# Kernel optimization log

Measured on AMD Instinct MI355X. Metric: run time of the kernel, lower is better.

Reference implementation:

```python
import jax, jax.numpy as jnp
import numpy as np
from jax import lax

DN = ('NHWC', 'HWIO', 'NHWC')

def conv2d(x, w, b):
    return lax.conv_general_dilated(x, w, (1, 1), 'SAME', dimension_numbers=DN) + b

def sdpa(q, k, v):
    # q,k,v: [B, C, L, D]; attend over L with feature dim D
    dk = jnp.asarray(q.shape[-1], dtype=q.dtype)
    scores = jnp.einsum('bcld,bcmd->bclm', q, k) / jnp.sqrt(dk)
    w = jax.nn.softmax(scores, axis=-1)
    return jnp.einsum('bclm,bcmd->bcld', w, v)

def setup_inputs() -> dict:
    key = jax.random.key(0)
    ks = jax.random.split(key, 8)
    B, T, F, N, C = 8, 512, 80, 64, 64
    s = 0.05
    return {
        'q': jax.random.normal(ks[0], (B, T, F, N), jnp.float32),
        'k': jax.random.normal(ks[1], (B, T, F, N), jnp.float32),
        'v': jax.random.normal(ks[2], (B, T, F, N), jnp.float32),
        'wq': jax.random.normal(ks[3], (3, 3, N, C), jnp.float32) * s,
        'bq': jnp.zeros((C,), jnp.float32),
        'wk': jax.random.normal(ks[4], (3, 3, N, C), jnp.float32) * s,
        'bk': jnp.zeros((C,), jnp.float32),
        'wv': jax.random.normal(ks[5], (3, 3, N, C), jnp.float32) * s,
        'bv': jnp.zeros((C,), jnp.float32),
        'wo': jax.random.normal(ks[6], (3, 3, 2 * C, N), jnp.float32) * s,
        'bo': jnp.zeros((N,), jnp.float32),
    }

def reference(q, k, v, wq, bq, wk, bk, wv, bv, wo, bo):
    cq = conv2d(q, wq, bq)  # [B,T,F,C]
    ck = conv2d(k, wk, bk)
    cv = conv2d(v, wv, bv)
    # 'freq' branch: [B,C,T,F], attention over T with feature dim F
    of = sdpa(jnp.transpose(cq, (0, 3, 1, 2)),
              jnp.transpose(ck, (0, 3, 1, 2)),
              jnp.transpose(cv, (0, 3, 1, 2)))  # [B,C,T,F]
    # 'time' branch: [B,C,F,T], attention over F with feature dim T
    ot = sdpa(jnp.transpose(cq, (0, 3, 2, 1)),
              jnp.transpose(ck, (0, 3, 2, 1)),
              jnp.transpose(cv, (0, 3, 2, 1)))  # [B,C,F,T]
    of = jnp.transpose(of, (0, 2, 3, 1))  # [B,T,F,C]
    ot = jnp.transpose(ot, (0, 3, 2, 1))  # [B,T,F,C]
    out = jnp.concatenate([ot, of], axis=-1)  # [B,T,F,2C]
    return conv2d(out, wo, bo)  # [B,T,F,N]
```

## Files before the change

kernel.cpp:

```cpp
#include <hip/hip_runtime.h>
#include <hip/hip_fp16.h>

#define TDIM 512
#define FDIM 80

typedef _Float16 f16x8 __attribute__((ext_vector_type(8)));
typedef _Float16 f16x4 __attribute__((ext_vector_type(4)));
typedef _Float16 f16x2 __attribute__((ext_vector_type(2)));
typedef float f32x4 __attribute__((ext_vector_type(4)));

__global__ __launch_bounds__(256) void k_prep_w(
    const float* __restrict__ wq, const float* __restrict__ wk,
    const float* __restrict__ wv, const float* __restrict__ wo,
    _Float16* __restrict__ wTq, _Float16* __restrict__ wTk,
    _Float16* __restrict__ wTv, _Float16* __restrict__ wTo)
{
  const int total = 3 * 36864 + 73728;
  for (int idx = blockIdx.x * 256 + threadIdx.x; idx < total; idx += gridDim.x * 256) {
    if (idx < 110592) {
      int sel = idx / 36864, r = idx - sel * 36864;
      int ci = r & 63, t2 = r >> 6, co = t2 & 63, kk = t2 >> 6;
      const float* src = (sel == 0) ? wq : (sel == 1) ? wk : wv;
      _Float16* dst = (sel == 0) ? wTq : (sel == 1) ? wTk : wTv;
      dst[r] = (_Float16)src[(kk * 64 + ci) * 64 + co];
    } else {
      int r = idx - 110592;
      int ci = r & 127, t2 = r >> 7, co = t2 & 63, kk = t2 >> 6;
      wTo[r] = (_Float16)wo[(kk * 128 + ci) * 64 + co];
    }
  }
}

__global__ __launch_bounds__(512) void k_conv_in3(
    const float* __restrict__ q, const float* __restrict__ k, const float* __restrict__ v,
    const float* __restrict__ wq, const float* __restrict__ wk, const float* __restrict__ wv,
    const _Float16* __restrict__ wTq, const _Float16* __restrict__ wTk, const _Float16* __restrict__ wTv,
    const float* __restrict__ bq, const float* __restrict__ bk, const float* __restrict__ bv,
    _Float16* __restrict__ yq, _Float16* __restrict__ yk, _Float16* __restrict__ yv)
{
  __shared__ __align__(16) _Float16 xs[328 * 72];
  const int bid = blockIdx.x;
  const int sel = bid >> 11, rest = bid & 2047;
  const float* x = (sel == 0) ? q : (sel == 1) ? k : v;
  const float* w = (sel == 0) ? wq : (sel == 1) ? wk : wv;
  const _Float16* wT = (sel == 0) ? wTq : (sel == 1) ? wTk : wTv;
  const float* bias = (sel == 0) ? bq : (sel == 1) ? bk : bv;
  _Float16* y = (sel == 0) ? yq : (sel == 1) ? yk : yv;

  const int xcd = rest & 7, i = rest >> 3;
  const int b = i >> 5, tp = i & 31;
  const int t0 = (xcd << 6) | (tp << 1);
  const int tid = threadIdx.x;
  const int wvv = tid >> 6, ln = tid & 63;
  const int tsel = wvv >> 2;
  const int lr = ln & 15, lg = ln >> 4;
  const int c0 = (wvv & 3) * 16;

  for (int idx = tid; idx < 328 * 16; idx += 512) {
    int r2 = idx >> 4, cq = idx & 15;
    int rr = r2 / 82, fi = r2 - rr * 82;
    int tt = t0 - 1 + rr, ff = fi - 1;
    f16x4 h;
    #pragma unroll
    for (int j = 0; j < 4; j++) h[j] = (_Float16)0.f;
    if (tt >= 0 && tt < TDIM && ff >= 0 && ff < FDIM) {
      float4 vv = *reinterpret_cast<const float4*>(x + (((b * TDIM + tt) * FDIM + ff) << 6) + cq * 4);
      h[0] = (_Float16)vv.x; h[1] = (_Float16)vv.y; h[2] = (_Float16)vv.z; h[3] = (_Float16)vv.w;
    }
    *reinterpret_cast<f16x4*>(&xs[r2 * 72 + cq * 4]) = h;
  }
  __syncthreads();

  float bvv = bias[c0 + lr];
  f32x4 acc[5];
  #pragma unroll
  for (int mt = 0; mt < 5; mt++)
    #pragma unroll
    for (int r = 0; r < 4; r++) acc[mt][r] = bvv;

  for (int ky = 0; ky < 3; ky++) {
    f16x8 wf[3][2];
    #pragma unroll
    for (int kx = 0; kx < 3; kx++)
      #pragma unroll
      for (int cc = 0; cc < 2; cc++) {
        if (wT) {
          wf[kx][cc] = *reinterpret_cast<const f16x8*>(
              wT + (((ky * 3 + kx) * 64 + c0 + lr) << 6) + cc * 32 + lg * 8);
        } else {
          const float* wp = w + ((ky * 3 + kx) * 64 + cc * 32 + lg * 8) * 64 + c0 + lr;
          #pragma unroll
          for (int j = 0; j < 8; j++) wf[kx][cc][j] = (_Float16)wp[j * 64];
        }
      }
    #pragma unroll
    for (int mt = 0; mt < 5; mt++) {
      #pragma unroll
      for (int kx = 0; kx < 3; kx++) {
        const _Float16* ap = &xs[((tsel + ky) * 82 + mt * 16 + lr + kx) * 72];
        #pragma unroll
        for (int cc = 0; cc < 2; cc++) {
          f16x8 af = *reinterpret_cast<const f16x8*>(ap + cc * 32 + lg * 8);
          acc[mt] = __builtin_amdgcn_mfma_f32_16x16x32_f16(af, wf[kx][cc], acc[mt], 0, 0, 0);
        }
      }
    }
  }

  __syncthreads();
  _Float16* yt = xs + tsel * 5632;
  const int c = c0 + lr;
  #pragma unroll
  for (int mt = 0; mt < 5; mt++) {
    f16x4 h;
    #pragma unroll
    for (int r = 0; r < 4; r++) h[r] = (_Float16)acc[mt][r];
    *reinterpret_cast<f16x4*>(&yt[c * 88 + mt * 16 + lg * 4]) = h;
  }
  __syncthreads();
  #pragma unroll
  for (int kk = 0; kk < 3; kk++) {
    int idx = tid + (kk << 9);
    if (idx < 1280) {
      int ts = idx >= 640, r2 = idx - ts * 640;
      int cc = r2 / 10, f8 = r2 - cc * 10;
      *reinterpret_cast<f16x8*>(y + ((size_t)(b * 64 + cc) * TDIM + t0 + ts) * FDIM + f8 * 8) =
          *reinterpret_cast<const f16x8*>(&xs[ts * 5632 + cc * 88 + f8 * 8]);
    }
  }
}

__global__ __launch_bounds__(512) void k_attn_freq(
    const _Float16* __restrict__ XQ, const _Float16* __restrict__ XK,
    const _Float16* __restrict__ XV, _Float16* __restrict__ CAT)
{
  __shared__ __align__(16) _Float16 Ks[64 * 104];
  __shared__ __align__(16) _Float16 Vt[96 * 72];
  __shared__ __align__(16) _Float16 Pl[8 * 16 * 72];

  const int bid = blockIdx.x;
  const int x8 = bid & 7, kk = bid >> 3;
  const int jj = kk & 7, tl = (kk >> 3) & 3, cc8 = kk >> 5;
  const int bc = x8 + cc8 * 64 + jj * 8;
  const int b = bc >> 6, c = bc & 63;
  const int t0 = tl * 128;
  const int tid = threadIdx.x;
  const int w8 = tid >> 6, ln = tid & 63;
  const int lr = ln & 15, lg = ln >> 4;
  const float qscale = 0.1118033988749895f;
  const float MFIX = 4.0f;

  const _Float16* Qg = XQ + (size_t)bc * 40960 + (size_t)t0 * 80;
  const _Float16* Kg = XK + (size_t)bc * 40960;
  const _Float16* Vg = XV + (size_t)bc * 40960;

  f16x8 qf[3];
  qf[0] = *reinterpret_cast<const f16x8*>(Qg + (w8 * 16 + lr) * 80 + lg * 8);
  qf[1] = *reinterpret_cast<const f16x8*>(Qg + (w8 * 16 + lr) * 80 + 32 + lg * 8);
  {
    f16x8 z;
    #pragma unroll
    for (int j = 0; j < 8; j++) z[j] = (_Float16)0.f;
    qf[2] = (lg < 2) ? *reinterpret_cast<const f16x8*>(Qg + (w8 * 16 + lr) * 80 + 64 + lg * 8) : z;
  }
  #pragma unroll
  for (int kc = 0; kc < 3; kc++)
    #pragma unroll
    for (int j = 0; j < 8; j++) qf[kc][j] = qf[kc][j] * (_Float16)qscale;

  if (tid < 192) {
    int row = tid / 3, cw = tid - row * 3;
    f16x8 z;
    #pragma unroll
    for (int j = 0; j < 8; j++) z[j] = (_Float16)0.f;
    *reinterpret_cast<f16x8*>(&Ks[row * 104 + 80 + cw * 8]) = z;
  }
  if (tid < 144) {
    int rr = tid / 9, cw = tid - rr * 9;
    int row = 80 + rr;
    f16x8 v;
    #pragma unroll
    for (int j = 0; j < 8; j++) v[j] = (row == 80) ? (_Float16)1.f : (_Float16)0.f;
    *reinterpret_cast<f16x8*>(&Vt[row * 72 + cw * 8]) = v;
  }

  const int vm = tid & 63;
  f16x8 kreg0, kreg1;
  f16x2 vreg[5];
  {
    int i0 = tid, r0 = i0 / 10, w0 = i0 - r0 * 10;
    kreg0 = *reinterpret_cast<const f16x8*>(Kg + r0 * 80 + w0 * 8);
    if (tid < 128) {
      int i1 = tid + 512, r1 = i1 / 10, w1 = i1 - r1 * 10;
      kreg1 = *reinterpret_cast<const f16x8*>(Kg + r1 * 80 + w1 * 8);
    }
    #pragma unroll
    for (int s = 0; s < 5; s++)
      vreg[s] = *reinterpret_cast<const f16x2*>(Vg + vm * 80 + (w8 + 8 * s) * 2);
  }

  f32x4 O[6];
  #pragma unroll
  for (int ft = 0; ft < 6; ft++)
    #pragma unroll
    for (int r = 0; r < 4; r++) O[ft][r] = 0.f;

  for (int kt = 0; kt < 8; kt++) {
    __syncthreads();
    {
      int i0 = tid, r0 = i0 / 10, w0 = i0 - r0 * 10;
      *reinterpret_cast<f16x8*>(&Ks[r0 * 104 + w0 * 8]) = kreg0;
      if (tid < 128) {
        int i1 = tid + 512, r1 = i1 / 10, w1 = i1 - r1 * 10;
        *reinterpret_cast<f16x8*>(&Ks[r1 * 104 + w1 * 8]) = kreg1;
      }
      #pragma unroll
      for (int s = 0; s < 5; s++) {
        int f2 = (w8 + 8 * s) * 2;
        Vt[f2 * 72 + vm]       = vreg[s][0];
        Vt[(f2 + 1) * 72 + vm] = vreg[s][1];
      }
    }
    if (kt < 7) {
      const _Float16* Kn = Kg + (kt + 1) * 64 * 80;
      const _Float16* Vn = Vg + (kt + 1) * 64 * 80;
      int i0 = tid, r0 = i0 / 10, w0 = i0 - r0 * 10;
      kreg0 = *reinterpret_cast<const f16x8*>(Kn + r0 * 80 + w0 * 8);
      if (tid < 128) {
        int i1 = tid + 512, r1 = i1 / 10, w1 = i1 - r1 * 10;
        kreg1 = *reinterpret_cast<const f16x8*>(Kn + r1 * 80 + w1 * 8);
      }
      #pragma unroll
      for (int s = 0; s < 5; s++)
        vreg[s] = *reinterpret_cast<const f16x2*>(Vn + vm * 80 + (w8 + 8 * s) * 2);
    }
    __syncthreads();

    f32x4 S[4];
    #pragma unroll
    for (int ms = 0; ms < 4; ms++)
      #pragma unroll
      for (int r = 0; r < 4; r++) S[ms][r] = 0.f;
    __builtin_amdgcn_s_setprio(1);
    #pragma unroll
    for (int kc = 0; kc < 3; kc++) {
      #pragma unroll
      for (int ms = 0; ms < 4; ms++) {
        f16x8 kf = *reinterpret_cast<const f16x8*>(&Ks[(ms * 16 + lr) * 104 + kc * 32 + lg * 8]);
        S[ms] = __builtin_amdgcn_mfma_f32_16x16x32_f16(qf[kc], kf, S[ms], 0, 0, 0);
      }
    }
    __builtin_amdgcn_s_setprio(0);

    _Float16* pw = &Pl[w8 * 16 * 72];
    #pragma unroll
    for (int r = 0; r < 4; r++) {
      int row = lg * 4 + r;
      #pragma unroll
      for (int ms = 0; ms < 4; ms++)
        pw[row * 72 + ((ms * 16 + lr) ^ (lg << 3))] = (_Float16)__expf(S[ms][r] - MFIX);
    }
    asm volatile("s_waitcnt lgkmcnt(0)" ::: "memory");
    const int sx = (lg ^ ((lr >> 2) & 3)) * 8;
    f16x8 pf0 = *reinterpret_cast<const f16x8*>(&pw[lr * 72 + sx]);
    f16x8 pf1 = *reinterpret_cast<const f16x8*>(&pw[lr * 72 + 32 + sx]);

    __builtin_amdgcn_s_setprio(1);
    #pragma unroll
    for (int ft = 0; ft < 6; ft++) {
      f16x8 vf0 = *reinterpret_cast<const f16x8*>(&Vt[(ft * 16 + lr) * 72 + lg * 8]);
      f16x8 vf1 = *reinterpret_cast<const f16x8*>(&Vt[(ft * 16 + lr) * 72 + 32 + lg * 8]);
      O[ft] = __builtin_amdgcn_mfma_f32_16x16x32_f16(pf0, vf0, O[ft], 0, 0, 0);
      O[ft] = __builtin_amdgcn_mfma_f32_16x16x32_f16(pf1, vf1, O[ft], 0, 0, 0);
    }
    __builtin_amdgcn_s_setprio(0);
  }

  float inv[4];
  #pragma unroll
  for (int r = 0; r < 4; r++) {
    float l = __shfl(O[5][r], lg << 4);
    inv[r] = 1.f / l;
  }
  #pragma unroll
  for (int r = 0; r < 4; r++) {
    int t = t0 + w8 * 16 + lg * 4 + r;
    size_t base = ((size_t)(b * 128 + 64 + c) * TDIM + t) * FDIM;
    #pragma unroll
    for (int ft = 0; ft < 5; ft++)
      CAT[base + ft * 16 + lr] = (_Float16)(O[ft][r] * inv[r]);
  }
}

__global__ __launch_bounds__(256) void k_attn_time(
    const _Float16* __restrict__ XQ, const _Float16* __restrict__ XK,
    const _Float16* __restrict__ XV, _Float16* __restrict__ CAT)
{
  __shared__ __align__(16) char smem[70400];
  _Float16* Qt  = (_Float16*)smem;
  _Float16* Kt  = Qt + 80 * 136;
  float*    Sld = (float*)(smem + 43520);
  _Float16* Pld = (_Float16*)smem;

  const int bid = blockIdx.x;
  const int b = bid >> 6, c = bid & 63;
  const int tid = threadIdx.x;
  const int wv = tid >> 6, ln = tid & 63;
  const int lr = ln & 15, lg = ln >> 4;
  const float tscale = 0.04419417382415922f;

  const _Float16* Qg = XQ + (size_t)bid * 40960;
  const _Float16* Kg = XK + (size_t)bid * 40960;
  const _Float16* Vg = XV + (size_t)bid * 40960;

  f32x4 sacc[7];
  #pragma unroll
  for (int i = 0; i < 7; i++)
    #pragma unroll
    for (int r = 0; r < 4; r++) sacc[i][r] = 0.f;

  for (int tc = 0; tc < 4; tc++) {
    __syncthreads();
    for (int idx = tid; idx < 640; idx += 256) {
      int t2 = idx / 10, f8 = idx - t2 * 10;
      int tg = tc * 128 + t2 * 2;
      f16x8 qa = *reinterpret_cast<const f16x8*>(Qg + (size_t)tg * 80 + f8 * 8);
      f16x8 qb = *reinterpret_cast<const f16x8*>(Qg + (size_t)(tg + 1) * 80 + f8 * 8);
      f16x8 ka = *reinterpret_cast<const f16x8*>(Kg + (size_t)tg * 80 + f8 * 8);
      f16x8 kb = *reinterpret_cast<const f16x8*>(Kg + (size_t)(tg + 1) * 80 + f8 * 8);
      #pragma unroll
      for (int j = 0; j < 8; j++) {
        int f = f8 * 8 + j;
        f16x2 qp; qp[0] = qa[j]; qp[1] = qb[j];
        f16x2 kp; kp[0] = ka[j]; kp[1] = kb[j];
        *reinterpret_cast<f16x2*>(&Qt[f * 136 + t2 * 2]) = qp;
        *reinterpret_cast<f16x2*>(&Kt[f * 136 + t2 * 2]) = kp;
      }
    }
    __syncthreads();
    #pragma unroll
    for (int i = 0; i < 7; i++) {
      int ti = wv * 7 + i;
      int te = ti < 25 ? ti : 24;
      int mi = te / 5, ni = te - mi * 5;
      #pragma unroll
      for (int kc = 0; kc < 4; kc++) {
        f16x8 aq = *reinterpret_cast<const f16x8*>(&Qt[(mi * 16 + lr) * 136 + kc * 32 + lg * 8]);
        f16x8 bk = *reinterpret_cast<const f16x8*>(&Kt[(ni * 16 + lr) * 136 + kc * 32 + lg * 8]);
        sacc[i] = __builtin_amdgcn_mfma_f32_16x16x32_f16(aq, bk, sacc[i], 0, 0, 0);
      }
    }
  }
  #pragma unroll
  for (int i = 0; i < 7; i++) {
    int ti = wv * 7 + i;
    if (ti < 25) {
      int mi = ti / 5, ni = ti - mi * 5;
      #pragma unroll
      for (int r = 0; r < 4; r++)
        Sld[(mi * 16 + lg * 4 + r) * 84 + ni * 16 + lr] = sacc[i][r] * tscale;
    }
  }
  __syncthreads();

  {
    const int fy = tid >> 4, gx = tid & 15;
    #pragma unroll
    for (int pass = 0; pass < 5; pass++) {
      int row = pass * 16 + fy;
      float s[5];
      #pragma unroll
      for (int j = 0; j < 5; j++) s[j] = Sld[row * 84 + gx + 16 * j];
      float mx = fmaxf(fmaxf(fmaxf(s[0], s[1]), fmaxf(s[2], s[3])), s[4]);
      #pragma unroll
      for (int sh = 1; sh < 16; sh <<= 1) mx = fmaxf(mx, __shfl_xor(mx, sh, 16));
      float e[5]; float ls = 0.f;
      #pragma unroll
      for (int j = 0; j < 5; j++) { e[j] = __expf(s[j] - mx); ls += e[j]; }
      #pragma unroll
      for (int sh = 1; sh < 16; sh <<= 1) ls += __shfl_xor(ls, sh, 16);
      float inv = 1.f / ls;
      #pragma unroll
      for (int j = 0; j < 5; j++)
        Pld[row * 104 + gx + 16 * j] = (_Float16)(e[j] * inv);
    }
    for (int idx = tid; idx < 240; idx += 256) {
      int row = idx / 3, cw = idx - row * 3;
      f16x8 z;
      #pragma unroll
      for (int j = 0; j < 8; j++) z[j] = (_Float16)0.f;
      *reinterpret_cast<f16x8*>(&Pld[row * 104 + 80 + cw * 8]) = z;
    }
  }
  __syncthreads();

  f16x8 pa[5][3];
  #pragma unroll
  for (int mi = 0; mi < 5; mi++)
    #pragma unroll
    for (int kc = 0; kc < 3; kc++)
      pa[mi][kc] = *reinterpret_cast<const f16x8*>(&Pld[(mi * 16 + lr) * 104 + kc * 32 + lg * 8]);

  _Float16* Ow = (_Float16*)(smem + 43520) + wv * (16 * 88);
  const size_t chbase = (size_t)(b * 128 + c) * TDIM * FDIM;

  #pragma unroll
  for (int j = 0; j < 8; j++) {
    int nt = wv * 8 + j;
    f16x8 vf[3];
    #pragma unroll
    for (int kc = 0; kc < 3; kc++) {
      if (kc < 2) {
        vf[kc] = *reinterpret_cast<const f16x8*>(Vg + (size_t)(nt * 16 + lr) * 80 + kc * 32 + lg * 8);
      } else {
        f16x8 z;
        #pragma unroll
        for (int q = 0; q < 8; q++) z[q] = (_Float16)0.f;
        vf[kc] = (lg < 2) ? *reinterpret_cast<const f16x8*>(Vg + (size_t)(nt * 16 + lr) * 80 + 64 + lg * 8) : z;
      }
    }
    f32x4 oacc[5];
    #pragma unroll
    for (int mi = 0; mi < 5; mi++)
      #pragma unroll
      for (int r = 0; r < 4; r++) oacc[mi][r] = 0.f;
    #pragma unroll
    for (int mi = 0; mi < 5; mi++)
      #pragma unroll
      for (int kc = 0; kc < 3; kc++)
        oacc[mi] = __builtin_amdgcn_mfma_f32_16x16x32_f16(pa[mi][kc], vf[kc], oacc[mi], 0, 0, 0);

    #pragma unroll
    for (int mi = 0; mi < 5; mi++) {
      f16x4 h;
      #pragma unroll
      for (int r = 0; r < 4; r++) h[r] = (_Float16)oacc[mi][r];
      *reinterpret_cast<f16x4*>(&Ow[lr * 88 + mi * 16 + lg * 4]) = h;
    }
    asm volatile("s_waitcnt lgkmcnt(0)" ::: "memory");
    size_t basec = chbase + (size_t)(nt * 16) * FDIM;
    #pragma unroll
    for (int k = 0; k < 3; k++) {
      int idx = ln + (k << 6);
      if (idx < 160) {
        int tl2 = idx / 10, f8 = idx - tl2 * 10;
        *reinterpret_cast<f16x8*>(CAT + basec + tl2 * 80 + f8 * 8) =
            *reinterpret_cast<const f16x8*>(&Ow[tl2 * 88 + f8 * 8]);
      }
    }
  }
}

__global__ __launch_bounds__(256) void k_conv_out(
    const _Float16* __restrict__ x, const float* __restrict__ w,
    const _Float16* __restrict__ wT,
    const float* __restrict__ bias, float* __restrict__ out)
{
  __shared__ __align__(16) _Float16 xs[246 * 72];
  const int bid = blockIdx.x;
  const int xcd = bid & 7, i = bid >> 3;
  const int b = i >> 6, t = (xcd << 6) | (i & 63);
  const int tid = threadIdx.x;
  const int wv = tid >> 6, ln = tid & 63;
  const int lr = ln & 15, lg = ln >> 4;
  const int c0 = wv * 16;

  float bv = bias[c0 + lr];
  f32x4 acc[5];
  #pragma unroll
  for (int mt = 0; mt < 5; mt++)
    #pragma unroll
    for (int r = 0; r < 4; r++) acc[mt][r] = bv;

  const _Float16* xb = x + (size_t)b * 128 * TDIM * FDIM;

  for (int h = 0; h < 2; h++) {
    __syncthreads();
    for (int idx = tid; idx < 384; idx += 256) {
      int cch = idx & 63, sk = idx >> 6;
      int ky = sk >> 1, side = sk & 1;
      xs[(ky * 82 + side * 81) * 72 + cch] = (_Float16)0.f;
    }
    #pragma unroll
    for (int k = 0; k < 8; k++) {
      int idx = tid + (k << 8);
      if (idx < 1920) {
        int cch = idx & 63, rest = idx >> 6;
        int ky = rest / 10, f8 = rest - ky * 10;
        int tt = t + ky - 1;
        f16x8 hh;
        #pragma unroll
        for (int j = 0; j < 8; j++) hh[j] = (_Float16)0.f;
        if (tt >= 0 && tt < TDIM)
          hh = *reinterpret_cast<const f16x8*>(xb + ((size_t)(h * 64 + cch) * TDIM + tt) * FDIM + f8 * 8);
        #pragma unroll
        for (int j = 0; j < 8; j++)
          xs[(ky * 82 + f8 * 8 + j + 1) * 72 + cch] = hh[j];
      }
    }
    __syncthreads();

    for (int ky = 0; ky < 3; ky++) {
      f16x8 wf[3][2];
      #pragma unroll
      for (int kx = 0; kx < 3; kx++)
        #pragma unroll
        for (int cc = 0; cc < 2; cc++) {
          if (wT) {
            wf[kx][cc] = *reinterpret_cast<const f16x8*>(
                wT + (((ky * 3 + kx) * 64 + c0 + lr) << 7) + h * 64 + cc * 32 + lg * 8);
          } else {
            const float* wp = w + ((ky * 3 + kx) * 128 + h * 64 + cc * 32 + lg * 8) * 64 + c0 + lr;
            #pragma unroll
            for (int j = 0; j < 8; j++) wf[kx][cc][j] = (_Float16)wp[j * 64];
          }
        }
      #pragma unroll
      for (int mt = 0; mt < 5; mt++) {
        #pragma unroll
        for (int kx = 0; kx < 3; kx++) {
          const _Float16* ap = &xs[(ky * 82 + mt * 16 + lr + kx) * 72];
          #pragma unroll
          for (int cc = 0; cc < 2; cc++) {
            f16x8 af = *reinterpret_cast<const f16x8*>(ap + cc * 32 + lg * 8);
            acc[mt] = __builtin_amdgcn_mfma_f32_16x16x32_f16(af, wf[kx][cc], acc[mt], 0, 0, 0);
          }
        }
      }
    }
  }

  const int c = c0 + lr;
  #pragma unroll
  for (int mt = 0; mt < 5; mt++) {
    #pragma unroll
    for (int r = 0; r < 4; r++) {
      int f = mt * 16 + lg * 4 + r;
      out[((size_t)(b * TDIM + t) * FDIM + f) * 64 + c] = acc[mt][r];
    }
  }
}

extern "C" void kernel_launch(void* const* d_in, const int* in_sizes, int n_in,
                              void* d_out, int out_size, void* d_ws, size_t ws_size,
                              hipStream_t stream)
{
  const float* q  = (const float*)d_in[0];
  const float* k  = (const float*)d_in[1];
  const float* v  = (const float*)d_in[2];
  const float* wq = (const float*)d_in[3];
  const float* bq = (const float*)d_in[4];
  const float* wk = (const float*)d_in[5];
  const float* bk = (const float*)d_in[6];
  const float* wv = (const float*)d_in[7];
  const float* bv = (const float*)d_in[8];
  const float* wo = (const float*)d_in[9];
  const float* bo = (const float*)d_in[10];

  const size_t PLANE = (size_t)8 * 64 * 512 * 80;
  _Float16* XQh  = (_Float16*)d_ws;
  _Float16* XKh  = XQh + PLANE;
  _Float16* CATh = XKh + PLANE;
  _Float16* XVh  = (_Float16*)d_out;

  _Float16* WT = CATh + 2 * PLANE;
  const size_t need = (4 * PLANE + 184320) * sizeof(_Float16);
  const bool useWT = (ws_size >= need);
  _Float16* wTq = useWT ? WT : nullptr;
  _Float16* wTk = useWT ? WT + 36864 : nullptr;
  _Float16* wTv = useWT ? WT + 73728 : nullptr;
  _Float16* wTo = useWT ? WT + 110592 : nullptr;

  if (useWT)
    hipLaunchKernelGGL(k_prep_w, dim3(180), dim3(256), 0, stream,
                       wq, wk, wv, wo, wTq, wTk, wTv, wTo);

  hipLaunchKernelGGL(k_conv_in3, dim3(6144), dim3(512), 0, stream,
                     q, k, v, wq, wk, wv, wTq, wTk, wTv, bq, bk, bv, XQh, XKh, XVh);
  hipLaunchKernelGGL(k_attn_freq, dim3(2048), dim3(512), 0, stream, XQh, XKh, XVh, CATh);
  hipLaunchKernelGGL(k_attn_time, dim3(512), dim3(256), 0, stream, XQh, XKh, XVh, CATh);
  hipLaunchKernelGGL(k_conv_out, dim3(4096), dim3(256), 0, stream, CATh, wo, wTo, bo, (float*)d_out);
}
```

Measured before the change: 402.8 us.

## Make input conv blocks loop over 16 time rows with rolling halo buffer

The input 3x3 convolution kernel now has each block process 16 consecutive time rows in 8 steps of two, keeping a 4-slot ring buffer of input rows in shared memory. Each step loads only the two new rows instead of reloading the full 4-row halo. This is meant to cut redundant global reads of overlapping input rows and amortize per-block setup, and the grid shrinks from 6144 to 768 blocks. In exchange, work inside each block is serialized across steps with two barriers per step, fewer blocks are available to hide latency, and loads are not overlapped with compute.

```diff
diff --git a/kernel.cpp b/kernel.cpp
--- a/kernel.cpp
+++ b/kernel.cpp
@@ -38,95 +38,123 @@
     const float* __restrict__ bq, const float* __restrict__ bk, const float* __restrict__ bv,
     _Float16* __restrict__ yq, _Float16* __restrict__ yk, _Float16* __restrict__ yv)
 {
-  __shared__ __align__(16) _Float16 xs[328 * 72];
+  __shared__ __align__(16) _Float16 xs[4 * 82 * 72];
+  __shared__ __align__(16) _Float16 bnc[2 * 5632];
+
   const int bid = blockIdx.x;
-  const int sel = bid >> 11, rest = bid & 2047;
+  const int xcd = bid & 7, r1 = bid >> 3;
+  const int sub = r1 & 3, r2b = r1 >> 2;
+  const int b = r2b & 7, sel = r2b >> 3;
   const float* x = (sel == 0) ? q : (sel == 1) ? k : v;
   const float* w = (sel == 0) ? wq : (sel == 1) ? wk : wv;
   const _Float16* wT = (sel == 0) ? wTq : (sel == 1) ? wTk : wTv;
   const float* bias = (sel == 0) ? bq : (sel == 1) ? bk : bv;
   _Float16* y = (sel == 0) ? yq : (sel == 1) ? yk : yv;
 
-  const int xcd = rest & 7, i = rest >> 3;
-  const int b = i >> 5, tp = i & 31;
-  const int t0 = (xcd << 6) | (tp << 1);
+  const int tbase = (xcd << 6) + (sub << 4);
   const int tid = threadIdx.x;
   const int wvv = tid >> 6, ln = tid & 63;
   const int tsel = wvv >> 2;
   const int lr = ln & 15, lg = ln >> 4;
   const int c0 = (wvv & 3) * 16;
 
-  for (int idx = tid; idx < 328 * 16; idx += 512) {
+  for (int idx = tid; idx < 4 * 82 * 16; idx += 512) {
     int r2 = idx >> 4, cq = idx & 15;
     int rr = r2 / 82, fi = r2 - rr * 82;
-    int tt = t0 - 1 + rr, ff = fi - 1;
+    int a = tbase - 1 + rr, ff = fi - 1;
     f16x4 h;
     #pragma unroll
     for (int j = 0; j < 4; j++) h[j] = (_Float16)0.f;
-    if (tt >= 0 && tt < TDIM && ff >= 0 && ff < FDIM) {
-      float4 vv = *reinterpret_cast<const float4*>(x + (((b * TDIM + tt) * FDIM + ff) << 6) + cq * 4);
+    if (a >= 0 && a < TDIM && ff >= 0 && ff < FDIM) {
+      float4 vv = *reinterpret_cast<const float4*>(x + (((b * TDIM + a) * FDIM + ff) << 6) + cq * 4);
       h[0] = (_Float16)vv.x; h[1] = (_Float16)vv.y; h[2] = (_Float16)vv.z; h[3] = (_Float16)vv.w;
     }
-    *reinterpret_cast<f16x4*>(&xs[r2 * 72 + cq * 4]) = h;
+    int slot = a & 3;
+    *reinterpret_cast<f16x4*>(&xs[(slot * 82 + fi) * 72 + cq * 4]) = h;
   }
   __syncthreads();
 
-  float bvv = bias[c0 + lr];
-  f32x4 acc[5];
-  #pragma unroll
-  for (int mt = 0; mt < 5; mt++)
-    #pragma unroll
-    for (int r = 0; r < 4; r++) acc[mt][r] = bvv;
-
-  for (int ky = 0; ky < 3; ky++) {
-    f16x8 wf[3][2];
-    #pragma unroll
-    for (int kx = 0; kx < 3; kx++)
-      #pragma unroll
-      for (int cc = 0; cc < 2; cc++) {
-        if (wT) {
-          wf[kx][cc] = *reinterpret_cast<const f16x8*>(
-              wT + (((ky * 3 + kx) * 64 + c0 + lr) << 6) + cc * 32 + lg * 8);
-        } else {
-          const float* wp = w + ((ky * 3 + kx) * 64 + cc * 32 + lg * 8) * 64 + c0 + lr;
+  const float bvv = bias[c0 + lr];
+
+  for (int p = 0; p < 8; p++) {
+    const int t = tbase + 2 * p + tsel;
+
+    f32x4 acc[5];
+    #pragma unroll
+    for (int mt = 0; mt < 5; mt++)
+      #pragma unroll
+      for (int r = 0; r < 4; r++) acc[mt][r] = bvv;
+
+    for (int ky = 0; ky < 3; ky++) {
+      const int slot = (t + ky - 1) & 3;
+      f16x8 wf[3][2];
+      #pragma unroll
+      for (int kx = 0; kx < 3; kx++)
+        #pragma unroll
+        for (int cc = 0; cc < 2; cc++) {
+          if (wT) {
+            wf[kx][cc] = *reinterpret_cast<const f16x8*>(
+                wT + (((ky * 3 + kx) * 64 + c0 + lr) << 6) + cc * 32 + lg * 8);
+          } else {
+            const float* wp = w + ((ky * 3 + kx) * 64 + cc * 32 + lg * 8) * 64 + c0 + lr;
+            #pragma unroll
+            for (int j = 0; j < 8; j++) wf[kx][cc][j] = (_Float16)wp[j * 64];
+          }
+        }
+      #pragma unroll
+      for (int mt = 0; mt < 5; mt++) {
+        #pragma unroll
+        for (int kx = 0; kx < 3; kx++) {
+          const _Float16* ap = &xs[(slot * 82 + mt * 16 + lr + kx) * 72];
           #pragma unroll
-          for (int j = 0; j < 8; j++) wf[kx][cc][j] = (_Float16)wp[j * 64];
+          for (int cc = 0; cc < 2; cc++) {
+            f16x8 af = *reinterpret_cast<const f16x8*>(ap + cc * 32 + lg * 8);
+            acc[mt] = __builtin_amdgcn_mfma_f32_16x16x32_f16(af, wf[kx][cc], acc[mt], 0, 0, 0);
+          }
         }
       }
-    #pragma unroll
-    for (int mt = 0; mt < 5; mt++) {
-      #pragma unroll
-      for (int kx = 0; kx < 3; kx++) {
-        const _Float16* ap = &xs[((tsel + ky) * 82 + mt * 16 + lr + kx) * 72];
-        #pragma unroll
-        for (int cc = 0; cc < 2; cc++) {
-          f16x8 af = *reinterpret_cast<const f16x8*>(ap + cc * 32 + lg * 8);
-          acc[mt] = __builtin_amdgcn_mfma_f32_16x16x32_f16(af, wf[kx][cc], acc[mt], 0, 0, 0);
+    }
+
+    {
+      _Float16* yt = bnc + tsel * 5632;
+      const int c = c0 + lr;
+      #pragma unroll
+      for (int mt = 0; mt < 5; mt++) {
+        f16x4 h;
+        #pragma unroll
+        for (int r = 0; r < 4; r++) h[r] = (_Float16)acc[mt][r];
+        *reinterpret_cast<f16x4*>(&yt[c * 88 + mt * 16 + lg * 4]) = h;
+      }
+    }
+    __syncthreads();
+
+    #pragma unroll
+    for (int kk = 0; kk < 3; kk++) {
+      int idx = tid + (kk << 9);
+      if (idx < 1280) {
+        int ts = idx >= 640, r2c = idx - ts * 640;
+        int cc = r2c / 10, f8 = r2c - cc * 10;
+        *reinterpret_cast<f16x8*>(y + ((size_t)(b * 64 + cc) * TDIM + tbase + 2 * p + ts) * FDIM + f8 * 8) =
+            *reinterpret_cast<const f16x8*>(&bnc[ts * 5632 + cc * 88 + f8 * 8]);
+      }
+    }
+    if (p < 7) {
+      for (int idx = tid; idx < 2 * 82 * 16; idx += 512) {
+        int r2c = idx >> 4, cq = idx & 15;
+        int rr = r2c / 82, fi = r2c - rr * 82;
+        int a = tbase + 2 * p + 3 + rr, ff = fi - 1;
+        f16x4 h;
+        #pragma unroll
+        for (int j = 0; j < 4; j++) h[j] = (_Float16)0.f;
+        if (a < TDIM && ff >= 0 && ff < FDIM) {
+          float4 vv = *reinterpret_cast<const float4*>(x + (((b * TDIM + a) * FDIM + ff) << 6) + cq * 4);
+          h[0] = (_Float16)vv.x; h[1] = (_Float16)vv.y; h[2] = (_Float16)vv.z; h[3] = (_Float16)vv.w;
         }
-      }
-    }
-  }
-
-  __syncthreads();
-  _Float16* yt = xs + tsel * 5632;
-  const int c = c0 + lr;
-  #pragma unroll
-  for (int mt = 0; mt < 5; mt++) {
-    f16x4 h;
-    #pragma unroll
-    for (int r = 0; r < 4; r++) h[r] = (_Float16)acc[mt][r];
-    *reinterpret_cast<f16x4*>(&yt[c * 88 + mt * 16 + lg * 4]) = h;
-  }
-  __syncthreads();
-  #pragma unroll
-  for (int kk = 0; kk < 3; kk++) {
-    int idx = tid + (kk << 9);
-    if (idx < 1280) {
-      int ts = idx >= 640, r2 = idx - ts * 640;
-      int cc = r2 / 10, f8 = r2 - cc * 10;
-      *reinterpret_cast<f16x8*>(y + ((size_t)(b * 64 + cc) * TDIM + t0 + ts) * FDIM + f8 * 8) =
-          *reinterpret_cast<const f16x8*>(&xs[ts * 5632 + cc * 88 + f8 * 8]);
-    }
+        int slot = a & 3;
+        *reinterpret_cast<f16x4*>(&xs[(slot * 82 + fi) * 72 + cq * 4]) = h;
+      }
+    }
+    __syncthreads();
   }
 }
 
@@ -415,7 +443,7 @@
       } else {
         f16x8 z;
         #pragma unroll
-        for (int q = 0; q < 8; q++) z[q] = (_Float16)0.f;
+        for (int qq = 0; qq < 8; qq++) z[qq] = (_Float16)0.f;
         vf[kc] = (lg < 2) ? *reinterpret_cast<const f16x8*>(Vg + (size_t)(nt * 16 + lr) * 80 + 64 + lg * 8) : z;
       }
     }
@@ -440,8 +468,8 @@
     asm volatile("s_waitcnt lgkmcnt(0)" ::: "memory");
     size_t basec = chbase + (size_t)(nt * 16) * FDIM;
     #pragma unroll
-    for (int k = 0; k < 3; k++) {
-      int idx = ln + (k << 6);
+    for (int kk2 = 0; kk2 < 3; kk2++) {
+      int idx = ln + (kk2 << 6);
       if (idx < 160) {
         int tl2 = idx / 10, f8 = idx - tl2 * 10;
         *reinterpret_cast<f16x8*>(CAT + basec + tl2 * 80 + f8 * 8) =
@@ -575,7 +603,7 @@
     hipLaunchKernelGGL(k_prep_w, dim3(180), dim3(256), 0, stream,
                        wq, wk, wv, wo, wTq, wTk, wTv, wTo);
 
-  hipLaunchKernelGGL(k_conv_in3, dim3(6144), dim3(512), 0, stream,
+  hipLaunchKernelGGL(k_conv_in3, dim3(768), dim3(512), 0, stream,
                      q, k, v, wq, wk, wv, wTq, wTk, wTv, bq, bk, bv, XQh, XKh, XVh);
   hipLaunchKernelGGL(k_attn_freq, dim3(2048), dim3(512), 0, stream, XQh, XKh, XVh, CATh);
   hipLaunchKernelGGL(k_attn_time, dim3(512), dim3(256), 0, stream, XQh, XKh, XVh, CATh);
```

Result: slower. 534.5 us (+32.7%).
